# Performance work log

Measured on AMD Instinct MI355X. Metric: run time of the kernel, lower is better.

## Reference

```python
import jax, jax.numpy as jnp
import numpy as np

N = 100000   # source points
M = 100000   # query (also) points
E = 2000000  # radius-neighbor pairs (row: query idx, col: source idx)
FEAT = 64
OUT = 2


def _linear_params(key, fan_in, fan_out):
    kw, kb = jax.random.split(key)
    bound = 1.0 / np.sqrt(fan_in)
    w = jax.random.uniform(kw, (fan_in, fan_out), jnp.float32, -bound, bound)
    b = jax.random.uniform(kb, (fan_out,), jnp.float32, -bound, bound)
    return w, b


def setup_inputs() -> dict:
    key = jax.random.key(0)
    ks = jax.random.split(key, 10)
    pcd = jax.random.normal(ks[0], (N, 3), jnp.float32)
    feats = jax.random.normal(ks[1], (N, FEAT), jnp.float32)
    also_pts = jax.random.normal(ks[2], (M, 3), jnp.float32)
    also_labels = jax.random.randint(ks[3], (M,), 0, 2, jnp.int64)
    row = jax.random.randint(ks[4], (E,), 0, M, jnp.int64)
    col = jax.random.randint(ks[5], (E,), 0, N, jnp.int64)
    w_in, b_in = _linear_params(ks[6], FEAT + 3, FEAT)
    w1, b1 = _linear_params(ks[7], FEAT, FEAT)
    w2, b2 = _linear_params(ks[8], FEAT, FEAT)
    w_out, b_out = _linear_params(ks[9], FEAT, OUT)
    return {"pcd": pcd, "feats": feats, "also_pts": also_pts,
            "also_labels": also_labels, "row": row, "col": col,
            "w_in": w_in, "b_in": b_in, "w1": w1, "b1": b1,
            "w2": w2, "b2": b2, "w_out": w_out, "b_out": b_out}


def reference(pcd, feats, also_pts, also_labels, row, col,
              w_in, b_in, w1, b1, w2, b2, w_out, b_out):
    # gather: relative position of query vs neighbor, and neighbor latent
    pos_relative = also_pts[row] - pcd[col]          # (E, 3)
    latents_relative = feats[col]                    # (E, FEAT)
    x = jnp.concatenate([latents_relative, pos_relative], axis=1)  # (E, FEAT+3)
    x = x @ w_in + b_in                              # fc_in
    x = jax.nn.relu(x) @ w1 + b1                     # mlp layer 0 (act then linear)
    x = jax.nn.relu(x) @ w2 + b2                     # mlp layer 1
    x = x @ w_out + b_out                            # fc_out -> (E, 2)
    probs = jax.nn.softmax(x, axis=1)
    return probs, also_labels[row]
```

## Files before the change

kernel.cpp:

```cpp
#include <hip/hip_runtime.h>
#include <hip/hip_bf16.h>


typedef _Float16 half8 __attribute__((ext_vector_type(8)));
typedef _Float16 half2v __attribute__((ext_vector_type(2)));
typedef __attribute__((ext_vector_type(4))) float f32x4;

union U84h { uint4 u; half8 h; };
union UW01 { uint4 u; _Float16 h[8]; };
union UPH  { half2v h; int i; };

__device__ __forceinline__ half8 relu8(half8 v) {
    half8 z;
#pragma unroll
    for (int i = 0; i < 8; ++i) z[i] = (_Float16)0.f;
    return __builtin_elementwise_max(v, z);
}
__device__ __forceinline__ half8 splat8(float v) {
    _Float16 h = (_Float16)v;
    half8 r = {h, h, h, h, h, h, h, h};
    return r;
}

__global__ __launch_bounds__(256) void pack_fold(
    const float* __restrict__ w1, const float* __restrict__ w_in,
    const float* __restrict__ b_in, const float* __restrict__ w2,
    const float* __restrict__ w_out, const float* __restrict__ b2,
    const float* __restrict__ b_out,
    _Float16* __restrict__ w1f, _Float16* __restrict__ wAf,
    _Float16* __restrict__ wpf, _Float16* __restrict__ bqf,
    _Float16* __restrict__ w01f, float* __restrict__ bf) {
    int t = blockIdx.x * 256 + threadIdx.x;
    if (t < 4096) {
        int f = t >> 9, lane = (t >> 3) & 63, j = t & 7;
        int ntile = f >> 1, kstep = f & 1;
        int k = kstep * 32 + ((lane >> 4) << 3) + j;
        int n = ntile * 16 + (lane & 15);
        w1f[t] = (_Float16)w1[k * 64 + n];
    } else if (t < 10240) {
        int i = t - 4096;
        int f = i >> 9, lane = (i >> 3) & 63, j = i & 7;
        int ntile = f / 3, ks = f % 3;
        int n = ntile * 16 + (lane & 15);
        float v;
        if (ks < 2) {
            int k = ks * 32 + ((lane >> 4) << 3) + j;
            v = w_in[k * 64 + n];
        } else {
            v = ((lane >> 4) == 0 && j < 3) ? -w_in[(64 + j) * 64 + n] : 0.f;
        }
        wAf[i] = (_Float16)v;
    } else if (t < 13312) {
        int i = t - 10240;
        int d = i >> 10, ks = (i >> 9) & 1, lane = (i >> 3) & 63, j = i & 7;
        int k = ks * 32 + ((lane >> 4) << 3) + j;
        wpf[i] = (_Float16)w_in[(64 + d) * 64 + k];
    } else if (t < 14336) {
        int i = t - 13312;
        int ks = i >> 9, lane = (i >> 3) & 63, j = i & 7;
        int k = ks * 32 + ((lane >> 4) << 3) + j;
        bqf[i] = (_Float16)b_in[k];
    } else if (t < 14400) {
        int n = t - 14336;
        float s0 = 0.f, s1 = 0.f;
#pragma unroll
        for (int j = 0; j < 64; ++j) {
            s0 = fmaf(w2[n * 64 + j], w_out[j * 2 + 0], s0);
            s1 = fmaf(w2[n * 64 + j], w_out[j * 2 + 1], s1);
        }
        w01f[2 * n]     = (_Float16)s0;
        w01f[2 * n + 1] = (_Float16)s1;
    } else if (t == 14400) {
        float s0 = b_out[0], s1 = b_out[1];
#pragma unroll
        for (int j = 0; j < 64; ++j) {
            s0 = fmaf(b2[j], w_out[j * 2 + 0], s0);
            s1 = fmaf(b2[j], w_out[j * 2 + 1], s1);
        }
        bf[0] = s0; bf[1] = s1;
    }
}

__global__ __launch_bounds__(256) void precompute_S(
    const float* __restrict__ feats, const float* __restrict__ pcd,
    const half8* __restrict__ wAf, _Float16* __restrict__ S, int N) {
    int lane = threadIdx.x & 63;
    int idx = lane & 15, g = lane >> 4;
    int base = (blockIdx.x * 4 + (threadIdx.x >> 6)) * 16;
    if (base >= N) return;

    half8 wa[12];
#pragma unroll
    for (int f = 0; f < 12; ++f) wa[f] = wAf[f * 64 + lane];

    int p = base + idx;
    int ps = p < N ? p : N - 1;
    const float4* fp = (const float4*)(feats + (size_t)ps * 64);
    float4 f0 = fp[2 * g], f1 = fp[2 * g + 1];
    float4 f2 = fp[8 + 2 * g], f3 = fp[8 + 2 * g + 1];
    half8 b0, b1, b2;
    b0[0]=(_Float16)f0.x; b0[1]=(_Float16)f0.y; b0[2]=(_Float16)f0.z; b0[3]=(_Float16)f0.w;
    b0[4]=(_Float16)f1.x; b0[5]=(_Float16)f1.y; b0[6]=(_Float16)f1.z; b0[7]=(_Float16)f1.w;
    b1[0]=(_Float16)f2.x; b1[1]=(_Float16)f2.y; b1[2]=(_Float16)f2.z; b1[3]=(_Float16)f2.w;
    b1[4]=(_Float16)f3.x; b1[5]=(_Float16)f3.y; b1[6]=(_Float16)f3.z; b1[7]=(_Float16)f3.w;
    float px = 0.f, py = 0.f, pz = 0.f;
    if (g == 0) {
        const float* pp = pcd + (size_t)ps * 3;
        px = pp[0]; py = pp[1]; pz = pp[2];
    }
#pragma unroll
    for (int i = 0; i < 8; ++i) b2[i] = (_Float16)0.f;
    b2[0] = (_Float16)px; b2[1] = (_Float16)py; b2[2] = (_Float16)pz;

    f32x4 zero = {0.f, 0.f, 0.f, 0.f};
#pragma unroll
    for (int tt = 0; tt < 4; ++tt) {
        f32x4 acc;
        acc = __builtin_amdgcn_mfma_f32_16x16x32_f16(wa[tt * 3 + 0], b0, zero, 0, 0, 0);
        acc = __builtin_amdgcn_mfma_f32_16x16x32_f16(wa[tt * 3 + 1], b1, acc, 0, 0, 0);
        acc = __builtin_amdgcn_mfma_f32_16x16x32_f16(wa[tt * 3 + 2], b2, acc, 0, 0, 0);
        union { uint2 u; _Float16 h[4]; } o;
        o.h[0] = (_Float16)acc[0]; o.h[1] = (_Float16)acc[1];
        o.h[2] = (_Float16)acc[2]; o.h[3] = (_Float16)acc[3];
        if (p < N) *(uint2*)(S + (size_t)p * 64 + tt * 16 + 4 * g) = o.u;
    }
}

__global__ __launch_bounds__(256, 4) void edge_mfma(
    const _Float16* __restrict__ S, const float* __restrict__ also_pts,
    const int* __restrict__ row, const int* __restrict__ col,
    const int* __restrict__ labels,
    const half8* __restrict__ w1f, const half8* __restrict__ wpf,
    const half8* __restrict__ bqf, const uint4* __restrict__ w01f,
    const float* __restrict__ bfold, const float* __restrict__ b1,
    float* __restrict__ out, int E, int ngroups) {
    __shared__ half8 wf_lds[8][64];
    {
        int t = threadIdx.x;
        wf_lds[t >> 6][t & 63] = w1f[t];
        wf_lds[(t + 256) >> 6][t & 63] = w1f[t + 256];
    }
    __syncthreads();

    int lane = threadIdx.x & 63;
    int idx  = lane & 15;
    int g    = lane >> 4;
    int gwave  = blockIdx.x * 4 + (threadIdx.x >> 6);
    int nwaves = gridDim.x * 4;

    half8 wpd[3][2];
#pragma unroll
    for (int d = 0; d < 3; ++d)
#pragma unroll
        for (int ks = 0; ks < 2; ++ks) wpd[d][ks] = wpf[(d * 2 + ks) * 64 + lane];
    half8 bq0 = bqf[lane], bq1 = bqf[64 + lane];
    uint4 w01v[4];
    f32x4 b1v[4];
#pragma unroll
    for (int tt = 0; tt < 4; ++tt) {
        w01v[tt] = w01f[tt * 4 + g];
        b1v[tt]  = *(const f32x4*)(b1 + tt * 16 + 4 * g);
    }
    float bf0 = bfold[0], bf1 = bfold[1];

    for (int grp = gwave; grp < ngroups; grp += nwaves) {
        int base = grp << 4;
        int e = base + idx;
        bool eok = (e < E);
        int es = eok ? e : (E - 1);
        int r = row[es];
        int c = col[es];

        const uint4* sp = (const uint4*)(S + (size_t)c * 64);
        U84h s0, s1;
        s0.u = sp[g];
        s1.u = sp[4 + g];
        const float* ap = also_pts + (size_t)r * 3;
        half8 axv = splat8(ap[0]), ayv = splat8(ap[1]), azv = splat8(ap[2]);
        half8 q0 = bq0 + axv * wpd[0][0] + ayv * wpd[1][0] + azv * wpd[2][0];
        half8 q1 = bq1 + axv * wpd[0][1] + ayv * wpd[1][1] + azv * wpd[2][1];
        half8 x0 = relu8(s0.h + q0);
        half8 x1 = relu8(s1.h + q1);

        f32x4 acc[4];
#pragma unroll
        for (int tt = 0; tt < 4; ++tt) {
            acc[tt] = __builtin_amdgcn_mfma_f32_16x16x32_f16(wf_lds[2 * tt][lane],     x0, b1v[tt], 0, 0, 0);
            acc[tt] = __builtin_amdgcn_mfma_f32_16x16x32_f16(wf_lds[2 * tt + 1][lane], x1, acc[tt], 0, 0, 0);
        }

        half2v p = {(_Float16)0.f, (_Float16)0.f};
#pragma unroll
        for (int tt = 0; tt < 4; ++tt) {
            UW01 wv; wv.u = w01v[tt];
#pragma unroll
            for (int reg = 0; reg < 4; ++reg) {
                _Float16 yh = (_Float16)fmaxf(acc[tt][reg], 0.f);
                half2v y2 = {yh, yh};
                half2v w2 = {wv.h[2 * reg], wv.h[2 * reg + 1]};
                p += y2 * w2;
            }
        }
        UPH pu; pu.h = p;
        UPH o;
        o.i = __shfl_xor(pu.i, 16); pu.h += o.h;
        o.i = __shfl_xor(pu.i, 32); pu.h += o.h;

        if (g == 0 && eok) {
            float l0 = (float)pu.h[0] + bf0;
            float l1 = (float)pu.h[1] + bf1;
            float mx = fmaxf(l0, l1);
            float e0 = __expf(l0 - mx);
            float e1 = __expf(l1 - mx);
            float inv = 1.f / (e0 + e1);
            *(float2*)(out + (size_t)e * 2) = make_float2(e0 * inv, e1 * inv);
            out[(size_t)2 * E + e] = (float)labels[r];
        }
    }
}

extern "C" void kernel_launch(void* const* d_in, const int* in_sizes, int n_in,
                              void* d_out, int out_size, void* d_ws, size_t ws_size,
                              hipStream_t stream) {
    const float* pcd      = (const float*)d_in[0];
    const float* feats    = (const float*)d_in[1];
    const float* also_pts = (const float*)d_in[2];
    const int*   labels   = (const int*)d_in[3];
    const int*   row      = (const int*)d_in[4];
    const int*   col      = (const int*)d_in[5];
    const float* w_in     = (const float*)d_in[6];
    const float* b_in     = (const float*)d_in[7];
    const float* w1       = (const float*)d_in[8];
    const float* b1       = (const float*)d_in[9];
    const float* w2       = (const float*)d_in[10];
    const float* b2       = (const float*)d_in[11];
    const float* w_out    = (const float*)d_in[12];
    const float* b_out    = (const float*)d_in[13];

    int N = in_sizes[0] / 3;
    int E = in_sizes[4];

    _Float16* Sb  = (_Float16*)d_ws;
    _Float16* w1f = Sb + (size_t)N * 64;
    _Float16* wAf = w1f + 4096;
    _Float16* wpf = wAf + 6144;
    _Float16* bqf = wpf + 3072;
    _Float16* w01 = bqf + 1024;
    float*    bf  = (float*)(w01 + 128);

    pack_fold<<<57, 256, 0, stream>>>(w1, w_in, b_in, w2, w_out, b2, b_out,
                                      w1f, wAf, wpf, bqf, w01, bf);

    int ngroupsS = (N + 15) / 16;
    precompute_S<<<(ngroupsS + 3) / 4, 256, 0, stream>>>(
        feats, pcd, (const half8*)wAf, Sb, N);

    int ngroups = (E + 15) / 16;
    edge_mfma<<<2048, 256, 0, stream>>>(Sb, also_pts, row, col, labels,
                                        (const half8*)w1f, (const half8*)wpf,
                                        (const half8*)bqf, (const uint4*)w01,
                                        bf, b1, (float*)d_out, E, ngroups);
}
```

Before: 84.63 us.

## Software-pipeline edge gathers and fold biases into packed-half epilogue

The edge loop now prefetches the next group's S rows, query coordinates and labels, and the row/col indices two groups ahead, so the dependent gather chain overlaps with the current group's MFMA work. The b_in bias moves into the precompute_S accumulator, which removes the per-edge bias add. The b1 bias and ReLU are applied in packed half after a pkrtz conversion, and the epilogue uses separate packed dot products for the two outputs. The trade-offs are more live registers, which could lower occupancy, and more arithmetic done in fp16.

```diff
diff --git a/kernel.cpp b/kernel.cpp
--- a/kernel.cpp
+++ b/kernel.cpp
@@ -4,11 +4,17 @@
 
 typedef _Float16 half8 __attribute__((ext_vector_type(8)));
 typedef _Float16 half2v __attribute__((ext_vector_type(2)));
+typedef __fp16   fp16x2 __attribute__((ext_vector_type(2)));
 typedef __attribute__((ext_vector_type(4))) float f32x4;
 
 union U84h { uint4 u; half8 h; };
-union UW01 { uint4 u; _Float16 h[8]; };
-union UPH  { half2v h; int i; };
+union UPH  { half2v h; fp16x2 f; int i; unsigned u; };
+
+__device__ __forceinline__ half2v cvt2h(float a, float b) {
+    UPH t;
+    t.f = __builtin_amdgcn_cvt_pkrtz(a, b);
+    return t.h;
+}
 
 __device__ __forceinline__ half8 relu8(half8 v) {
     half8 z;
@@ -16,20 +22,16 @@
     for (int i = 0; i < 8; ++i) z[i] = (_Float16)0.f;
     return __builtin_elementwise_max(v, z);
 }
-__device__ __forceinline__ half8 splat8(float v) {
-    _Float16 h = (_Float16)v;
-    half8 r = {h, h, h, h, h, h, h, h};
-    return r;
-}
 
 __global__ __launch_bounds__(256) void pack_fold(
     const float* __restrict__ w1, const float* __restrict__ w_in,
-    const float* __restrict__ b_in, const float* __restrict__ w2,
+    const float* __restrict__ b1, const float* __restrict__ w2,
     const float* __restrict__ w_out, const float* __restrict__ b2,
     const float* __restrict__ b_out,
     _Float16* __restrict__ w1f, _Float16* __restrict__ wAf,
-    _Float16* __restrict__ wpf, _Float16* __restrict__ bqf,
-    _Float16* __restrict__ w01f, float* __restrict__ bf) {
+    _Float16* __restrict__ wpf, _Float16* __restrict__ w0h,
+    _Float16* __restrict__ w1h, _Float16* __restrict__ b1h,
+    float* __restrict__ bf) {
     int t = blockIdx.x * 256 + threadIdx.x;
     if (t < 4096) {
         int f = t >> 9, lane = (t >> 3) & 63, j = t & 7;
@@ -55,22 +57,20 @@
         int d = i >> 10, ks = (i >> 9) & 1, lane = (i >> 3) & 63, j = i & 7;
         int k = ks * 32 + ((lane >> 4) << 3) + j;
         wpf[i] = (_Float16)w_in[(64 + d) * 64 + k];
-    } else if (t < 14336) {
-        int i = t - 13312;
-        int ks = i >> 9, lane = (i >> 3) & 63, j = i & 7;
-        int k = ks * 32 + ((lane >> 4) << 3) + j;
-        bqf[i] = (_Float16)b_in[k];
-    } else if (t < 14400) {
-        int n = t - 14336;
+    } else if (t < 13376) {
+        int n = t - 13312;
         float s0 = 0.f, s1 = 0.f;
 #pragma unroll
         for (int j = 0; j < 64; ++j) {
             s0 = fmaf(w2[n * 64 + j], w_out[j * 2 + 0], s0);
             s1 = fmaf(w2[n * 64 + j], w_out[j * 2 + 1], s1);
         }
-        w01f[2 * n]     = (_Float16)s0;
-        w01f[2 * n + 1] = (_Float16)s1;
-    } else if (t == 14400) {
+        w0h[n] = (_Float16)s0;
+        w1h[n] = (_Float16)s1;
+    } else if (t < 13440) {
+        int n = t - 13376;
+        b1h[n] = (_Float16)b1[n];
+    } else if (t == 13440) {
         float s0 = b_out[0], s1 = b_out[1];
 #pragma unroll
         for (int j = 0; j < 64; ++j) {
@@ -83,7 +83,8 @@
 
 __global__ __launch_bounds__(256) void precompute_S(
     const float* __restrict__ feats, const float* __restrict__ pcd,
-    const half8* __restrict__ wAf, _Float16* __restrict__ S, int N) {
+    const float* __restrict__ b_in, const half8* __restrict__ wAf,
+    _Float16* __restrict__ S, int N) {
     int lane = threadIdx.x & 63;
     int idx = lane & 15, g = lane >> 4;
     int base = (blockIdx.x * 4 + (threadIdx.x >> 6)) * 16;
@@ -98,27 +99,27 @@
     const float4* fp = (const float4*)(feats + (size_t)ps * 64);
     float4 f0 = fp[2 * g], f1 = fp[2 * g + 1];
     float4 f2 = fp[8 + 2 * g], f3 = fp[8 + 2 * g + 1];
-    half8 b0, b1, b2;
+    half8 b0, b1v, b2v;
     b0[0]=(_Float16)f0.x; b0[1]=(_Float16)f0.y; b0[2]=(_Float16)f0.z; b0[3]=(_Float16)f0.w;
     b0[4]=(_Float16)f1.x; b0[5]=(_Float16)f1.y; b0[6]=(_Float16)f1.z; b0[7]=(_Float16)f1.w;
-    b1[0]=(_Float16)f2.x; b1[1]=(_Float16)f2.y; b1[2]=(_Float16)f2.z; b1[3]=(_Float16)f2.w;
-    b1[4]=(_Float16)f3.x; b1[5]=(_Float16)f3.y; b1[6]=(_Float16)f3.z; b1[7]=(_Float16)f3.w;
+    b1v[0]=(_Float16)f2.x; b1v[1]=(_Float16)f2.y; b1v[2]=(_Float16)f2.z; b1v[3]=(_Float16)f2.w;
+    b1v[4]=(_Float16)f3.x; b1v[5]=(_Float16)f3.y; b1v[6]=(_Float16)f3.z; b1v[7]=(_Float16)f3.w;
     float px = 0.f, py = 0.f, pz = 0.f;
     if (g == 0) {
         const float* pp = pcd + (size_t)ps * 3;
         px = pp[0]; py = pp[1]; pz = pp[2];
     }
 #pragma unroll
-    for (int i = 0; i < 8; ++i) b2[i] = (_Float16)0.f;
-    b2[0] = (_Float16)px; b2[1] = (_Float16)py; b2[2] = (_Float16)pz;
-
-    f32x4 zero = {0.f, 0.f, 0.f, 0.f};
+    for (int i = 0; i < 8; ++i) b2v[i] = (_Float16)0.f;
+    b2v[0] = (_Float16)px; b2v[1] = (_Float16)py; b2v[2] = (_Float16)pz;
+
 #pragma unroll
     for (int tt = 0; tt < 4; ++tt) {
+        f32x4 bi = *(const f32x4*)(b_in + tt * 16 + 4 * g);
         f32x4 acc;
-        acc = __builtin_amdgcn_mfma_f32_16x16x32_f16(wa[tt * 3 + 0], b0, zero, 0, 0, 0);
-        acc = __builtin_amdgcn_mfma_f32_16x16x32_f16(wa[tt * 3 + 1], b1, acc, 0, 0, 0);
-        acc = __builtin_amdgcn_mfma_f32_16x16x32_f16(wa[tt * 3 + 2], b2, acc, 0, 0, 0);
+        acc = __builtin_amdgcn_mfma_f32_16x16x32_f16(wa[tt * 3 + 0], b0, bi, 0, 0, 0);
+        acc = __builtin_amdgcn_mfma_f32_16x16x32_f16(wa[tt * 3 + 1], b1v, acc, 0, 0, 0);
+        acc = __builtin_amdgcn_mfma_f32_16x16x32_f16(wa[tt * 3 + 2], b2v, acc, 0, 0, 0);
         union { uint2 u; _Float16 h[4]; } o;
         o.h[0] = (_Float16)acc[0]; o.h[1] = (_Float16)acc[1];
         o.h[2] = (_Float16)acc[2]; o.h[3] = (_Float16)acc[3];
@@ -131,8 +132,8 @@
     const int* __restrict__ row, const int* __restrict__ col,
     const int* __restrict__ labels,
     const half8* __restrict__ w1f, const half8* __restrict__ wpf,
-    const half8* __restrict__ bqf, const uint4* __restrict__ w01f,
-    const float* __restrict__ bfold, const float* __restrict__ b1,
+    const unsigned* __restrict__ w0p, const unsigned* __restrict__ w1p,
+    const unsigned* __restrict__ b1p, const float* __restrict__ bfold,
     float* __restrict__ out, int E, int ngroups) {
     __shared__ half8 wf_lds[8][64];
     {
@@ -147,75 +148,101 @@
     int g    = lane >> 4;
     int gwave  = blockIdx.x * 4 + (threadIdx.x >> 6);
     int nwaves = gridDim.x * 4;
+    if (gwave >= ngroups) return;
 
     half8 wpd[3][2];
 #pragma unroll
     for (int d = 0; d < 3; ++d)
 #pragma unroll
         for (int ks = 0; ks < 2; ++ks) wpd[d][ks] = wpf[(d * 2 + ks) * 64 + lane];
-    half8 bq0 = bqf[lane], bq1 = bqf[64 + lane];
-    uint4 w01v[4];
-    f32x4 b1v[4];
-#pragma unroll
-    for (int tt = 0; tt < 4; ++tt) {
-        w01v[tt] = w01f[tt * 4 + g];
-        b1v[tt]  = *(const f32x4*)(b1 + tt * 16 + 4 * g);
-    }
+    UPH w0v[8], w1v[8], b1v[8];
+#pragma unroll
+    for (int tt = 0; tt < 4; ++tt)
+#pragma unroll
+        for (int h = 0; h < 2; ++h) {
+            int i = tt * 8 + 2 * g + h;
+            w0v[tt * 2 + h].u = w0p[i];
+            w1v[tt * 2 + h].u = w1p[i];
+            b1v[tt * 2 + h].u = b1p[i];
+        }
     float bf0 = bfold[0], bf1 = bfold[1];
-
-    for (int grp = gwave; grp < ngroups; grp += nwaves) {
-        int base = grp << 4;
-        int e = base + idx;
-        bool eok = (e < E);
-        int es = eok ? e : (E - 1);
-        int r = row[es];
-        int c = col[es];
-
-        const uint4* sp = (const uint4*)(S + (size_t)c * 64);
-        U84h s0, s1;
-        s0.u = sp[g];
-        s1.u = sp[4 + g];
-        const float* ap = also_pts + (size_t)r * 3;
-        half8 axv = splat8(ap[0]), ayv = splat8(ap[1]), azv = splat8(ap[2]);
-        half8 q0 = bq0 + axv * wpd[0][0] + ayv * wpd[1][0] + azv * wpd[2][0];
-        half8 q1 = bq1 + axv * wpd[0][1] + ayv * wpd[1][1] + azv * wpd[2][1];
-        half8 x0 = relu8(s0.h + q0);
-        half8 x1 = relu8(s1.h + q1);
-
+    half2v zero2 = {(_Float16)0.f, (_Float16)0.f};
+
+    int grp = gwave, stride = nwaves;
+    int es0 = (grp << 4) + idx; es0 = es0 < E ? es0 : E - 1;
+    int r_c = row[es0], c_c = col[es0];
+    const uint4* sp0 = (const uint4*)(S + (size_t)c_c * 64);
+    uint4 s0_c = sp0[g], s1_c = sp0[4 + g];
+    const float* ap0 = also_pts + (size_t)r_c * 3;
+    float ax_c = ap0[0], ay_c = ap0[1], az_c = ap0[2];
+    int lb_c = labels[r_c];
+
+    int gn = grp + stride; gn = gn < ngroups ? gn : grp;
+    int es1 = (gn << 4) + idx; es1 = es1 < E ? es1 : E - 1;
+    int r_n = row[es1], c_n = col[es1];
+
+    for (; grp < ngroups; grp += stride) {
+        const uint4* spn = (const uint4*)(S + (size_t)c_n * 64);
+        uint4 s0_n = spn[g], s1_n = spn[4 + g];
+        const float* apn = also_pts + (size_t)r_n * 3;
+        float ax_n = apn[0], ay_n = apn[1], az_n = apn[2];
+        int lb_n = labels[r_n];
+        int g2 = grp + 2 * stride; g2 = g2 < ngroups ? g2 : grp;
+        int es2 = (g2 << 4) + idx; es2 = es2 < E ? es2 : E - 1;
+        int r_2 = row[es2], c_2 = col[es2];
+
+        int e = (grp << 4) + idx;
+        bool eok = e < E;
+        U84h s0u, s1u; s0u.u = s0_c; s1u.u = s1_c;
+        _Float16 ah = (_Float16)ax_c, bh = (_Float16)ay_c, ch = (_Float16)az_c;
+        half8 av = {ah, ah, ah, ah, ah, ah, ah, ah};
+        half8 bv = {bh, bh, bh, bh, bh, bh, bh, bh};
+        half8 cv = {ch, ch, ch, ch, ch, ch, ch, ch};
+        half8 q0 = av * wpd[0][0] + bv * wpd[1][0] + cv * wpd[2][0];
+        half8 q1 = av * wpd[0][1] + bv * wpd[1][1] + cv * wpd[2][1];
+        half8 x0 = relu8(s0u.h + q0);
+        half8 x1 = relu8(s1u.h + q1);
+
+        f32x4 zero = {0.f, 0.f, 0.f, 0.f};
         f32x4 acc[4];
 #pragma unroll
         for (int tt = 0; tt < 4; ++tt) {
-            acc[tt] = __builtin_amdgcn_mfma_f32_16x16x32_f16(wf_lds[2 * tt][lane],     x0, b1v[tt], 0, 0, 0);
+            acc[tt] = __builtin_amdgcn_mfma_f32_16x16x32_f16(wf_lds[2 * tt][lane],     x0, zero, 0, 0, 0);
             acc[tt] = __builtin_amdgcn_mfma_f32_16x16x32_f16(wf_lds[2 * tt + 1][lane], x1, acc[tt], 0, 0, 0);
         }
 
-        half2v p = {(_Float16)0.f, (_Float16)0.f};
+        half2v p0 = zero2, p1 = zero2;
 #pragma unroll
         for (int tt = 0; tt < 4; ++tt) {
-            UW01 wv; wv.u = w01v[tt];
-#pragma unroll
-            for (int reg = 0; reg < 4; ++reg) {
-                _Float16 yh = (_Float16)fmaxf(acc[tt][reg], 0.f);
-                half2v y2 = {yh, yh};
-                half2v w2 = {wv.h[2 * reg], wv.h[2 * reg + 1]};
-                p += y2 * w2;
-            }
-        }
-        UPH pu; pu.h = p;
-        UPH o;
-        o.i = __shfl_xor(pu.i, 16); pu.h += o.h;
-        o.i = __shfl_xor(pu.i, 32); pu.h += o.h;
+            half2v h01 = cvt2h(acc[tt][0], acc[tt][1]);
+            half2v h23 = cvt2h(acc[tt][2], acc[tt][3]);
+            h01 = __builtin_elementwise_max(h01 + b1v[tt * 2 + 0].h, zero2);
+            h23 = __builtin_elementwise_max(h23 + b1v[tt * 2 + 1].h, zero2);
+            p0 += h01 * w0v[tt * 2 + 0].h + h23 * w0v[tt * 2 + 1].h;
+            p1 += h01 * w1v[tt * 2 + 0].h + h23 * w1v[tt * 2 + 1].h;
+        }
+        UPH P0, P1, T;
+        P0.h = p0; P1.h = p1;
+        T.i = __shfl_xor(P0.i, 16); P0.h += T.h;
+        T.i = __shfl_xor(P0.i, 32); P0.h += T.h;
+        T.i = __shfl_xor(P1.i, 16); P1.h += T.h;
+        T.i = __shfl_xor(P1.i, 32); P1.h += T.h;
 
         if (g == 0 && eok) {
-            float l0 = (float)pu.h[0] + bf0;
-            float l1 = (float)pu.h[1] + bf1;
+            float l0 = (float)P0.h[0] + (float)P0.h[1] + bf0;
+            float l1 = (float)P1.h[0] + (float)P1.h[1] + bf1;
             float mx = fmaxf(l0, l1);
             float e0 = __expf(l0 - mx);
             float e1 = __expf(l1 - mx);
             float inv = 1.f / (e0 + e1);
             *(float2*)(out + (size_t)e * 2) = make_float2(e0 * inv, e1 * inv);
-            out[(size_t)2 * E + e] = (float)labels[r];
-        }
+            out[(size_t)2 * E + e] = (float)lb_c;
+        }
+
+        s0_c = s0_n; s1_c = s1_n;
+        ax_c = ax_n; ay_c = ay_n; az_c = az_n;
+        lb_c = lb_n;
+        r_n = r_2; c_n = c_2;
     }
 }
 
@@ -244,20 +271,22 @@
     _Float16* w1f = Sb + (size_t)N * 64;
     _Float16* wAf = w1f + 4096;
     _Float16* wpf = wAf + 6144;
-    _Float16* bqf = wpf + 3072;
-    _Float16* w01 = bqf + 1024;
-    float*    bf  = (float*)(w01 + 128);
-
-    pack_fold<<<57, 256, 0, stream>>>(w1, w_in, b_in, w2, w_out, b2, b_out,
-                                      w1f, wAf, wpf, bqf, w01, bf);
+    _Float16* w0h = wpf + 3072;
+    _Float16* w1h = w0h + 64;
+    _Float16* b1h = w1h + 64;
+    float*    bf  = (float*)(b1h + 64);
+
+    pack_fold<<<53, 256, 0, stream>>>(w1, w_in, b1, w2, w_out, b2, b_out,
+                                      w1f, wAf, wpf, w0h, w1h, b1h, bf);
 
     int ngroupsS = (N + 15) / 16;
     precompute_S<<<(ngroupsS + 3) / 4, 256, 0, stream>>>(
-        feats, pcd, (const half8*)wAf, Sb, N);
+        feats, pcd, b_in, (const half8*)wAf, Sb, N);
 
     int ngroups = (E + 15) / 16;
     edge_mfma<<<2048, 256, 0, stream>>>(Sb, also_pts, row, col, labels,
                                         (const half8*)w1f, (const half8*)wpf,
-                                        (const half8*)bqf, (const uint4*)w01,
-                                        bf, b1, (float*)d_out, E, ngroups);
-}
+                                        (const unsigned*)w0h, (const unsigned*)w1h,
+                                        (const unsigned*)b1h, bf,
+                                        (float*)d_out, E, ngroups);
+}
```

Result: faster. 81.83 us (-3.3%).
